# Kernel optimization log

Measured on AMD Instinct MI355X. Metric: run time of the kernel, lower is better.

## Reference

```python
import jax, jax.numpy as jnp
import numpy as np

DIMS = (50000, 50000)
ORDER = len(DIMS)
NUM_FEATS = 64
QLEVEL = 4
Q = 1 << QLEVEL
V = 1 << ORDER                      # number of corners (2^order)
N_QUERIES = 1_000_000
WHICH_AXIS = np.repeat(np.arange(ORDER), DIMS)          # [sum(dims)]
OFFSETS = np.concatenate([[0], np.cumsum(DIMS)[:-1]])   # row offset of each axis in feats
# corner bit table: flattening of a [2]*order grid is row-major, so axis i's bit is (v >> (ORDER-1-i)) & 1
VBITS = (np.arange(V)[:, None] >> (ORDER - 1 - np.arange(ORDER))[None, :]) & 1  # [V, ORDER]


def setup_inputs() -> dict:
    key = jax.random.key(0)
    k = jax.random.split(key, 8)
    S = sum(DIMS)
    init_scale = 0.01 / NUM_FEATS ** 0.5
    values = jax.random.truncated_normal(k[0], -2.0, 2.0, (1, V, NUM_FEATS), dtype=jnp.float32) * init_scale
    feats = jax.random.uniform(k[1], (S, NUM_FEATS), dtype=jnp.float32)
    lo = 1.0 / (1 << (QLEVEL + 1))
    cand_row = jnp.linspace(lo, 1.0 - lo, Q, dtype=jnp.float32).reshape(1, 1, Q)
    candidates = jnp.tile(cand_row, (ORDER, NUM_FEATS, 1))
    scale = jnp.zeros((1,), jnp.float32)
    bias = jnp.zeros((1,), jnp.float32)
    idx0 = jax.random.randint(k[2], (N_QUERIES,), 0, DIMS[0])
    idx1 = jax.random.randint(k[3], (N_QUERIES,), 0, DIMS[1])
    return {"values": values, "feats": feats, "candidates": candidates,
            "scale": scale, "bias": bias, "idx0": idx0, "idx1": idx1}


def reference(values, feats, candidates, scale, bias, idx0, idx1):
    # --- prepare_inputs: straight-through quantization of feats ---
    target_keys = candidates[WHICH_AXIS]                                  # [S, F, Q]
    assigned = jnp.argmin(jnp.abs(feats[:, :, None] - target_keys), -1)   # [S, F]
    qkeys = jnp.take_along_axis(target_keys, assigned[:, :, None], -1)[..., 0]  # [S, F]
    probs = qkeys + feats - jax.lax.stop_gradient(feats)                  # STE
    p = jnp.stack([probs, 1.0 - probs], 0)                                # [2, S, F]

    # --- per-axis gathers ---
    idxs = [idx0, idx1]
    gathers = [p[:, OFFSETS[i] + idxs[i]] for i in range(ORDER)]          # each [2, N, F]

    # --- corner-wise outer product across axes ---
    corner = gathers[0][VBITS[:, 0]]                                      # [V, N, F]
    for i in range(1, ORDER):
        corner = corner * gathers[i][VBITS[:, i]]

    # --- contraction with corner values, halve features, tanh gate ---
    t = jnp.einsum('vf,vnf->nf', values[0], corner)                       # [N, F]
    half = NUM_FEATS // 2
    a = t[:, :half].sum(-1)                                               # [N]
    b = t[:, half:].sum(-1)                                               # [N]
    return a * jnp.tanh(b) * jnp.exp(scale[0]) + bias[0]
```

## Files before the change

kernel.cpp:

```cpp
#include <hip/hip_runtime.h>
#include <stdint.h>

#define NF    64
#define DIM0  50000
#define SROWS 100000
#define TPB   256
#define COEF_OFF_BYTES (SROWS * 32)

typedef float    f32x4 __attribute__((ext_vector_type(4)));
typedef uint32_t u32x4 __attribute__((ext_vector_type(4)));

__global__ void quantize_kernel(const float* __restrict__ feats,
                                const float* __restrict__ values,
                                uint32_t* __restrict__ qcodes,
                                float* __restrict__ coef) {
    int t = threadIdx.x;
    if (blockIdx.x == 0 && t < NF) {
        float v0 = values[t], v1 = values[NF + t];
        float v2 = values[2 * NF + t], v3 = values[3 * NF + t];
        float W = v0 - v1 - v2 + v3;
        float X = v1 - v3, Y = v2 - v3;
        float Wp = W * (1.0f / 256.0f);
        float Xp = W * (1.0f / 512.0f) + X * (1.0f / 16.0f);
        float Yp = W * (1.0f / 512.0f) + Y * (1.0f / 16.0f);
        float C  = W * (1.0f / 1024.0f) + (X + Y) * (1.0f / 32.0f) + v3;
        ((f32x4*)coef)[t] = (f32x4){Wp, Xp, Yp, C};
        float Cs = C;
        Cs += __shfl_xor(Cs, 1);  Cs += __shfl_xor(Cs, 2);
        Cs += __shfl_xor(Cs, 4);  Cs += __shfl_xor(Cs, 8);
        Cs += __shfl_xor(Cs, 16);
        if (t == 0)  coef[NF * 4 + 0] = Cs;
        if (t == 32) coef[NF * 4 + 1] = Cs;
    }

    int gid = blockIdx.x * blockDim.x + t;
    const f32x4* fr = (const f32x4*)(feats + (size_t)gid * 8);
    f32x4 fA = __builtin_nontemporal_load(fr);
    f32x4 fB = __builtin_nontemporal_load(fr + 1);
    float fv[8] = {fA.x, fA.y, fA.z, fA.w, fB.x, fB.y, fB.z, fB.w};

    uint32_t word = 0u;
#pragma unroll
    for (int j = 0; j < 8; ++j) {
        float x = fmaf(fv[j], 16.0f, -1.0f);
        int q = (int)ceilf(x);
        q = q < 0 ? 0 : (q > 15 ? 15 : q);
        word |= (uint32_t)q << (4 * j);
    }
    qcodes[gid] = word;
}

__global__ __launch_bounds__(TPB) void query_kernel(
        const uint32_t* __restrict__ qcodes,
        const f32x4* __restrict__ coef,
        const float* __restrict__ scale,
        const float* __restrict__ bias,
        const int* __restrict__ idx0,
        const int* __restrict__ idx1,
        float* __restrict__ out, int N) {
    int n = blockIdx.x * TPB + threadIdx.x;
    if (n >= N) return;

    int r0 = __builtin_nontemporal_load(idx0 + n);
    int r1 = DIM0 + __builtin_nontemporal_load(idx1 + n);

    const u32x4* pa = (const u32x4*)(qcodes + (size_t)r0 * 8);
    const u32x4* pb = (const u32x4*)(qcodes + (size_t)r1 * 8);
    u32x4 x0 = pa[0], x1 = pa[1];
    u32x4 y0 = pb[0], y1 = pb[1];
    uint32_t aw[8] = {x0.x, x0.y, x0.z, x0.w, x1.x, x1.y, x1.z, x1.w};
    uint32_t bw[8] = {y0.x, y0.y, y0.z, y0.w, y1.x, y1.y, y1.z, y1.w};

    float crA = 0.f, crB = 0.f;
    float lAa = 0.f, lAb = 0.f;
    float lBa = 0.f, lBb = 0.f;
#pragma unroll
    for (int wd = 0; wd < 8; ++wd) {
        uint32_t wa = aw[wd];
        uint32_t wb = bw[wd];
#pragma unroll
        for (int j = 0; j < 8; ++j) {
            int f = wd * 8 + j;
            f32x4 c = coef[f];
            float Af = (float)((wa >> (4 * j)) & 15u);
            float Bf = (float)((wb >> (4 * j)) & 15u);
            float pf = Af * Bf;
            if (wd < 4) {
                crA = fmaf(pf, c.x, crA);
                lAa = fmaf(Af, c.y, lAa);
                lBa = fmaf(Bf, c.z, lBa);
            } else {
                crB = fmaf(pf, c.x, crB);
                lAb = fmaf(Af, c.y, lAb);
                lBb = fmaf(Bf, c.z, lBb);
            }
        }
    }

    const float* cs = (const float*)coef;
    float Ca = cs[NF * 4 + 0];
    float Cb = cs[NF * 4 + 1];
    float es = expf(scale[0]);
    float bi = bias[0];
    float asum = crA + lAa + lBa + Ca;
    float bsum = crB + lAb + lBb + Cb;
    __builtin_nontemporal_store(asum * tanhf(bsum) * es + bi, out + n);
}

extern "C" void kernel_launch(void* const* d_in, const int* in_sizes, int n_in,
                              void* d_out, int out_size, void* d_ws, size_t ws_size,
                              hipStream_t stream) {
    const float* values = (const float*)d_in[0];
    const float* feats  = (const float*)d_in[1];
    const float* scale  = (const float*)d_in[3];
    const float* bias   = (const float*)d_in[4];
    const int*   idx0   = (const int*)d_in[5];
    const int*   idx1   = (const int*)d_in[6];
    float*       out    = (float*)d_out;

    uint32_t* qcodes = (uint32_t*)d_ws;
    float*    coef   = (float*)((char*)d_ws + COEF_OFF_BYTES);

    int nwords = SROWS * 8;
    quantize_kernel<<<nwords / TPB, TPB, 0, stream>>>(feats, values, qcodes, coef);

    int N = out_size;
    query_kernel<<<(N + TPB - 1) / TPB, TPB, 0, stream>>>(
        qcodes, (const f32x4*)coef, scale, bias, idx0, idx1, out, N);
}
```

Baseline: 36.09 us.

## Split each query across two lanes, one per feature half, combine via shuffle

Each query is now handled by two lanes of a wavefront, one for each 32-feature half. Each lane does one 16-byte gather per axis instead of two and half the FMAs, and the halves are combined with a cross-lane shuffle before the tanh gate. This doubles the thread count and adds per-lane selects between two coefficient sets. Idx loads are duplicated across the lane pair. The aim is more memory-level parallelism and shorter per-thread dependency chains.

```diff
diff --git a/kernel.cpp b/kernel.cpp
--- a/kernel.cpp
+++ b/kernel.cpp
@@ -58,53 +58,54 @@
         const int* __restrict__ idx0,
         const int* __restrict__ idx1,
         float* __restrict__ out, int N) {
-    int n = blockIdx.x * TPB + threadIdx.x;
-    if (n >= N) return;
+    int t    = threadIdx.x;
+    int lane = t & 63;
+    int wid  = t >> 6;
+    int q    = lane & 31;
+    int h    = lane >> 5;
 
-    int r0 = __builtin_nontemporal_load(idx0 + n);
-    int r1 = DIM0 + __builtin_nontemporal_load(idx1 + n);
+    int qi = blockIdx.x * (TPB / 64 * 32) + wid * 32 + q;
+    int m  = qi < N ? qi : N - 1;
 
-    const u32x4* pa = (const u32x4*)(qcodes + (size_t)r0 * 8);
-    const u32x4* pb = (const u32x4*)(qcodes + (size_t)r1 * 8);
-    u32x4 x0 = pa[0], x1 = pa[1];
-    u32x4 y0 = pb[0], y1 = pb[1];
-    uint32_t aw[8] = {x0.x, x0.y, x0.z, x0.w, x1.x, x1.y, x1.z, x1.w};
-    uint32_t bw[8] = {y0.x, y0.y, y0.z, y0.w, y1.x, y1.y, y1.z, y1.w};
+    int r0 = idx0[m];
+    int r1 = DIM0 + idx1[m];
 
-    float crA = 0.f, crB = 0.f;
-    float lAa = 0.f, lAb = 0.f;
-    float lBa = 0.f, lBb = 0.f;
+    u32x4 va = *((const u32x4*)(qcodes + (size_t)r0 * 8) + h);
+    u32x4 vb = *((const u32x4*)(qcodes + (size_t)r1 * 8) + h);
+    uint32_t aw[4] = {va.x, va.y, va.z, va.w};
+    uint32_t bw[4] = {vb.x, vb.y, vb.z, vb.w};
+
+    bool hi = (h != 0);
+    float acc = 0.0f;
 #pragma unroll
-    for (int wd = 0; wd < 8; ++wd) {
+    for (int wd = 0; wd < 4; ++wd) {
         uint32_t wa = aw[wd];
         uint32_t wb = bw[wd];
 #pragma unroll
         for (int j = 0; j < 8; ++j) {
             int f = wd * 8 + j;
-            f32x4 c = coef[f];
-            float Af = (float)((wa >> (4 * j)) & 15u);
-            float Bf = (float)((wb >> (4 * j)) & 15u);
-            float pf = Af * Bf;
-            if (wd < 4) {
-                crA = fmaf(pf, c.x, crA);
-                lAa = fmaf(Af, c.y, lAa);
-                lBa = fmaf(Bf, c.z, lBa);
-            } else {
-                crB = fmaf(pf, c.x, crB);
-                lAb = fmaf(Af, c.y, lAb);
-                lBb = fmaf(Bf, c.z, lBb);
-            }
+            f32x4 cA = coef[f];
+            f32x4 cB = coef[32 + f];
+            float Wp = hi ? cB.x : cA.x;
+            float Xp = hi ? cB.y : cA.y;
+            float Yp = hi ? cB.z : cA.z;
+            float A = (float)((wa >> (4 * j)) & 15u);
+            float B = (float)((wb >> (4 * j)) & 15u);
+            acc = fmaf(A, fmaf(Wp, B, Xp), fmaf(Yp, B, acc));
         }
     }
 
     const float* cs = (const float*)coef;
     float Ca = cs[NF * 4 + 0];
     float Cb = cs[NF * 4 + 1];
-    float es = expf(scale[0]);
-    float bi = bias[0];
-    float asum = crA + lAa + lBa + Ca;
-    float bsum = crB + lAb + lBb + Cb;
-    __builtin_nontemporal_store(asum * tanhf(bsum) * es + bi, out + n);
+    acc += hi ? Cb : Ca;
+
+    float other = __shfl_xor(acc, 32);
+    if (h == 0 && qi < N) {
+        float es = expf(scale[0]);
+        float bi2 = bias[0];
+        __builtin_nontemporal_store(acc * tanhf(other) * es + bi2, out + qi);
+    }
 }
 
 extern "C" void kernel_launch(void* const* d_in, const int* in_sizes, int n_in,
@@ -125,6 +126,8 @@
     quantize_kernel<<<nwords / TPB, TPB, 0, stream>>>(feats, values, qcodes, coef);
 
     int N = out_size;
-    query_kernel<<<(N + TPB - 1) / TPB, TPB, 0, stream>>>(
+    int qpb = TPB / 64 * 32;
+    int qblocks = (N + qpb - 1) / qpb;
+    query_kernel<<<qblocks, TPB, 0, stream>>>(
         qcodes, (const f32x4*)coef, scale, bias, idx0, idx1, out, N);
 }
```

New measurement: 36.89 us. +2.2%, slower.

## Use packed fp16 dot products for query math and a grid-stride query loop

Applied to the files above, without the earlier changes.

Coefficients are stored as packed fp16 pairs, pre-scaled by 4096, in a matching interleaved order. The query kernel turns the 4-bit codes into fp16 with a magic-number trick and accumulates with v_dot2 (fdot2) instead of scalar float FMAs, which cuts ALU instruction count. It also switches to a fixed 2048-block grid-stride loop so the scale, bias and constant loads are hoisted out of the per-query work. In exchange, fp16 coefficients and products lose precision. The products stay exact since they are at most 225, but the coefficient rounding could hurt accuracy.

```diff
diff --git a/kernel.cpp b/kernel.cpp
--- a/kernel.cpp
+++ b/kernel.cpp
@@ -5,35 +5,66 @@
 #define DIM0  50000
 #define SROWS 100000
 #define TPB   256
+#define QBLKS 3125
+#define QGRID 2048
 #define COEF_OFF_BYTES (SROWS * 32)
 
 typedef float    f32x4 __attribute__((ext_vector_type(4)));
 typedef uint32_t u32x4 __attribute__((ext_vector_type(4)));
+typedef __fp16   h16x2 __attribute__((ext_vector_type(2)));
 
-__global__ void quantize_kernel(const float* __restrict__ feats,
-                                const float* __restrict__ values,
-                                uint32_t* __restrict__ qcodes,
-                                float* __restrict__ coef) {
+#if __has_builtin(__builtin_amdgcn_fdot2)
+#define FDOT2(a, b, c) __builtin_amdgcn_fdot2((a), (b), (c), false)
+#else
+static __device__ inline float FDOT2(h16x2 a, h16x2 b, float c) {
+    return fmaf((float)a.x, (float)b.x, fmaf((float)a.y, (float)b.y, c));
+}
+#endif
+
+
+__global__ __launch_bounds__(TPB) void quantize_kernel(
+        const float* __restrict__ feats, const float* __restrict__ values,
+        uint32_t* __restrict__ qcodes, uint32_t* __restrict__ coef) {
     int t = threadIdx.x;
     if (blockIdx.x == 0 && t < NF) {
         float v0 = values[t], v1 = values[NF + t];
         float v2 = values[2 * NF + t], v3 = values[3 * NF + t];
         float W = v0 - v1 - v2 + v3;
         float X = v1 - v3, Y = v2 - v3;
-        float Wp = W * (1.0f / 256.0f);
-        float Xp = W * (1.0f / 512.0f) + X * (1.0f / 16.0f);
-        float Yp = W * (1.0f / 512.0f) + Y * (1.0f / 16.0f);
-        float C  = W * (1.0f / 1024.0f) + (X + Y) * (1.0f / 32.0f) + v3;
-        ((f32x4*)coef)[t] = (f32x4){Wp, Xp, Yp, C};
+        float C = W * (1.0f / 1024.0f) + (X + Y) * (1.0f / 32.0f) + v3;
         float Cs = C;
         Cs += __shfl_xor(Cs, 1);  Cs += __shfl_xor(Cs, 2);
         Cs += __shfl_xor(Cs, 4);  Cs += __shfl_xor(Cs, 8);
         Cs += __shfl_xor(Cs, 16);
-        if (t == 0)  coef[NF * 4 + 0] = Cs;
-        if (t == 32) coef[NF * 4 + 1] = Cs;
+        if (t == 0)  ((float*)coef)[96] = Cs;
+        if (t == 32) ((float*)coef)[97] = Cs;
+
+        if (t < 32) {
+            int flo = (t >> 2) * 8 + (t & 3);
+            int fhi = flo + 4;
+#pragma unroll
+            for (int which = 0; which < 3; ++which) {
+                float clo, chi;
+#pragma unroll
+                for (int pick = 0; pick < 2; ++pick) {
+                    int f = pick ? fhi : flo;
+                    float w0 = values[f], w1 = values[NF + f];
+                    float w2v = values[2 * NF + f], w3 = values[3 * NF + f];
+                    float Wf = w0 - w1 - w2v + w3;
+                    float Xf = w1 - w3, Yf = w2v - w3;
+                    float c;
+                    if (which == 0)      c = Wf * (4096.0f / 256.0f);
+                    else if (which == 1) c = (Wf * (1.0f/512.0f) + Xf * (1.0f/16.0f)) * 4096.0f;
+                    else                 c = (Wf * (1.0f/512.0f) + Yf * (1.0f/16.0f)) * 4096.0f;
+                    if (pick) chi = c; else clo = c;
+                }
+                h16x2 p = {(__fp16)clo, (__fp16)chi};
+                coef[which * 32 + t] = __builtin_bit_cast(uint32_t, p);
+            }
+        }
     }
 
-    int gid = blockIdx.x * blockDim.x + t;
+    int gid = blockIdx.x * TPB + t;
     const f32x4* fr = (const f32x4*)(feats + (size_t)gid * 8);
     f32x4 fA = __builtin_nontemporal_load(fr);
     f32x4 fB = __builtin_nontemporal_load(fr + 1);
@@ -52,59 +83,62 @@
 
 __global__ __launch_bounds__(TPB) void query_kernel(
         const uint32_t* __restrict__ qcodes,
-        const f32x4* __restrict__ coef,
+        const uint32_t* __restrict__ coef,
         const float* __restrict__ scale,
         const float* __restrict__ bias,
         const int* __restrict__ idx0,
         const int* __restrict__ idx1,
         float* __restrict__ out, int N) {
-    int n = blockIdx.x * TPB + threadIdx.x;
-    if (n >= N) return;
+    int t = threadIdx.x;
+    float es = expf(scale[0]);
+    float bi = bias[0];
+    float Ca = ((const float*)coef)[96];
+    float Cb = ((const float*)coef)[97];
 
-    int r0 = __builtin_nontemporal_load(idx0 + n);
-    int r1 = DIM0 + __builtin_nontemporal_load(idx1 + n);
+    for (int n = blockIdx.x * TPB + t; n < N; n += QGRID * TPB) {
+        int r0 = __builtin_nontemporal_load(idx0 + n);
+        int r1 = DIM0 + __builtin_nontemporal_load(idx1 + n);
 
-    const u32x4* pa = (const u32x4*)(qcodes + (size_t)r0 * 8);
-    const u32x4* pb = (const u32x4*)(qcodes + (size_t)r1 * 8);
-    u32x4 x0 = pa[0], x1 = pa[1];
-    u32x4 y0 = pb[0], y1 = pb[1];
-    uint32_t aw[8] = {x0.x, x0.y, x0.z, x0.w, x1.x, x1.y, x1.z, x1.w};
-    uint32_t bw[8] = {y0.x, y0.y, y0.z, y0.w, y1.x, y1.y, y1.z, y1.w};
+        const u32x4* pa = (const u32x4*)(qcodes + (size_t)r0 * 8);
+        const u32x4* pb = (const u32x4*)(qcodes + (size_t)r1 * 8);
+        u32x4 x0 = pa[0], x1 = pa[1];
+        u32x4 y0 = pb[0], y1 = pb[1];
+        uint32_t aw[8] = {x0.x, x0.y, x0.z, x0.w, x1.x, x1.y, x1.z, x1.w};
+        uint32_t bw[8] = {y0.x, y0.y, y0.z, y0.w, y1.x, y1.y, y1.z, y1.w};
 
-    float crA = 0.f, crB = 0.f;
-    float lAa = 0.f, lAb = 0.f;
-    float lBa = 0.f, lBb = 0.f;
+        float cc_a = 0.f, ca_a = 0.f, cb_a = 0.f;
+        float cc_b = 0.f, ca_b = 0.f, cb_b = 0.f;
+        const h16x2 k1024 = {(__fp16)1024.0f, (__fp16)1024.0f};
 #pragma unroll
-    for (int wd = 0; wd < 8; ++wd) {
-        uint32_t wa = aw[wd];
-        uint32_t wb = bw[wd];
+        for (int wd = 0; wd < 8; ++wd) {
+            uint32_t wa = aw[wd];
+            uint32_t wb = bw[wd];
 #pragma unroll
-        for (int j = 0; j < 8; ++j) {
-            int f = wd * 8 + j;
-            f32x4 c = coef[f];
-            float Af = (float)((wa >> (4 * j)) & 15u);
-            float Bf = (float)((wb >> (4 * j)) & 15u);
-            float pf = Af * Bf;
-            if (wd < 4) {
-                crA = fmaf(pf, c.x, crA);
-                lAa = fmaf(Af, c.y, lAa);
-                lBa = fmaf(Bf, c.z, lBa);
-            } else {
-                crB = fmaf(pf, c.x, crB);
-                lAb = fmaf(Af, c.y, lAb);
-                lBb = fmaf(Bf, c.z, lBb);
+            for (int j = 0; j < 4; ++j) {
+                uint32_t ua = ((wa >> (4 * j)) & 0x000F000Fu) | 0x64006400u;
+                uint32_t ub = ((wb >> (4 * j)) & 0x000F000Fu) | 0x64006400u;
+                h16x2 a2 = __builtin_bit_cast(h16x2, ua) - k1024;
+                h16x2 b2 = __builtin_bit_cast(h16x2, ub) - k1024;
+                h16x2 ab = a2 * b2;
+                h16x2 w2 = __builtin_bit_cast(h16x2, coef[wd * 4 + j]);
+                h16x2 x2 = __builtin_bit_cast(h16x2, coef[32 + wd * 4 + j]);
+                h16x2 y2 = __builtin_bit_cast(h16x2, coef[64 + wd * 4 + j]);
+                if (wd < 4) {
+                    cc_a = FDOT2(w2, ab, cc_a);
+                    ca_a = FDOT2(x2, a2, ca_a);
+                    cb_a = FDOT2(y2, b2, cb_a);
+                } else {
+                    cc_b = FDOT2(w2, ab, cc_b);
+                    ca_b = FDOT2(x2, a2, ca_b);
+                    cb_b = FDOT2(y2, b2, cb_b);
+                }
             }
         }
+
+        float asum = (cc_a + ca_a + cb_a) * (1.0f / 4096.0f) + Ca;
+        float bsum = (cc_b + ca_b + cb_b) * (1.0f / 4096.0f) + Cb;
+        __builtin_nontemporal_store(asum * tanhf(bsum) * es + bi, out + n);
     }
-
-    const float* cs = (const float*)coef;
-    float Ca = cs[NF * 4 + 0];
-    float Cb = cs[NF * 4 + 1];
-    float es = expf(scale[0]);
-    float bi = bias[0];
-    float asum = crA + lAa + lBa + Ca;
-    float bsum = crB + lAb + lBb + Cb;
-    __builtin_nontemporal_store(asum * tanhf(bsum) * es + bi, out + n);
 }
 
 extern "C" void kernel_launch(void* const* d_in, const int* in_sizes, int n_in,
@@ -119,12 +153,11 @@
     float*       out    = (float*)d_out;
 
     uint32_t* qcodes = (uint32_t*)d_ws;
-    float*    coef   = (float*)((char*)d_ws + COEF_OFF_BYTES);
+    uint32_t* coef   = (uint32_t*)((char*)d_ws + COEF_OFF_BYTES);
 
-    int nwords = SROWS * 8;
-    quantize_kernel<<<nwords / TPB, TPB, 0, stream>>>(feats, values, qcodes, coef);
+    quantize_kernel<<<QBLKS, TPB, 0, stream>>>(feats, values, qcodes, coef);
 
     int N = out_size;
-    query_kernel<<<(N + TPB - 1) / TPB, TPB, 0, stream>>>(
-        qcodes, (const f32x4*)coef, scale, bias, idx0, idx1, out, N);
+    query_kernel<<<QGRID, TPB, 0, stream>>>(
+        qcodes, coef, scale, bias, idx0, idx1, out, N);
 }
```

New measurement: 35.84 us. No clear change (-0.7%).
